# Performance work log

Measured on AMD Instinct MI355X. Metric: run time of the kernel, lower is better.

## Reference

```python
import jax, jax.numpy as jnp
import numpy as np


def setup_inputs() -> dict:
    key = jax.random.key(0)
    k1, k2, k3 = jax.random.split(key, 3)
    x = jax.random.normal(k1, (32, 256, 32, 32), dtype=jnp.float32)
    weight = jax.random.normal(k2, (256, 256, 3, 3), dtype=jnp.float32) * 0.05
    bias = jax.random.normal(k3, (256,), dtype=jnp.float32) * 0.01
    return {"x": x, "weight": weight, "bias": bias}


def _forward(x, weight, bias):
    B, cin, n, _ = x.shape
    cout, _, k, _ = weight.shape
    s = (k - 1) // 2
    nf = n // 2 + 1
    bins = n * nf

    # fft shift matrix: exp(-1j*2*pi*s*(i+j)/n), kept rfft columns
    idx = jnp.arange(n)
    shift = idx[None, :] + idx[:, None]                     # (n, n)
    shift_m = jnp.exp(-1j * 2 * jnp.pi * s * shift / n)[:, :nf]
    shift_m = shift_m.reshape(bins, 1, 1).astype(jnp.complex64)

    # xfft: (B, cin, n, nf) -> (bins, cin, B)
    xfft = jnp.fft.rfft2(x)
    xfft = jnp.transpose(xfft, (2, 3, 1, 0)).reshape(bins, cin, B)

    # Hfft: (cout, cin, n, nf) -> (bins, cout, cin), shifted + conj
    Hfft = jnp.fft.rfft2(weight, s=(n, n)).reshape(cout, cin, bins)
    Hfft = shift_m * jnp.conj(jnp.transpose(Hfft, (2, 0, 1)))

    def sq_abs(z):
        return jnp.real(z) ** 2 + jnp.imag(z) ** 2

    RowNorm = jnp.sqrt(jnp.sum(sq_abs(Hfft), axis=2))       # (bins, cout)
    ColNorm = jnp.sqrt(jnp.sum(sq_abs(Hfft), axis=1))       # (bins, cin)

    if cout >= cin:
        RowLoss = jnp.mean((RowNorm - jnp.sqrt(cin / cout)) ** 2)
        ColLoss = jnp.mean((ColNorm - 1.0) ** 2)
        HHT = jnp.einsum('npc,nqc->npq', jnp.conj(Hfft), Hfft)  # (bins, cout, cout)
        mask = jnp.triu(jnp.ones((cout, cout), bool), k=1)
        count = bins * (cout * (cout - 1) // 2)
        AngLoss = jnp.sum(sq_abs(HHT) * mask[None]) / count   # MSE(|HHT[triu]|, 0)
        L = cout * ColLoss + cin * RowLoss + AngLoss
    else:
        RowLoss = jnp.mean((RowNorm - 1.0) ** 2)
        ColLoss = jnp.mean((ColNorm - jnp.sqrt(cout / cin)) ** 2)
        HTH = jnp.einsum('ndp,ndq->npq', jnp.conj(Hfft), Hfft)  # (bins, cin, cin)
        mask = jnp.triu(jnp.ones((cin, cin), bool), k=1)
        count = bins * (cin * (cin - 1) // 2)
        AngLoss = jnp.sum(sq_abs(HTH) * mask[None]) / count
        L = cout * ColLoss + cin * RowLoss + AngLoss

    # per-bin complex matmul: (bins, cout, cin) @ (bins, cin, B) -> (bins, cout, B)
    yfft = Hfft @ xfft
    yfft = jnp.transpose(yfft.reshape(n, nf, cout, B), (3, 2, 0, 1))  # (B, cout, n, nf)
    y = jnp.fft.irfft2(yfft, s=(n, n))
    y = y + bias[None, :, None, None]
    return y, L


def reference(x, weight, bias):
    return _forward(x, weight, bias)
```

## Files before the change

kernel.cpp:

```cpp
#include <hip/hip_runtime.h>
#include <math.h>

typedef __attribute__((ext_vector_type(8)))  short  short8;
typedef __attribute__((ext_vector_type(16))) float  float16;

#define TWO_PI_OVER_32 0.19634954084936207f

static __device__ __forceinline__ unsigned short f2bf(float f) {
    unsigned int u = __float_as_uint(f);
    u = (u + 0x7FFFu + ((u >> 16) & 1u)) >> 16;
    return (unsigned short)u;
}
static __device__ __forceinline__ float bf2f(unsigned short s) {
    return __uint_as_float(((unsigned int)s) << 16);
}

static __device__ __forceinline__ void g2l16(const void* g, void* l) {
    __builtin_amdgcn_global_load_lds(
        (const __attribute__((address_space(1))) unsigned int*)g,
        (__attribute__((address_space(3))) unsigned int*)l, 16, 0, 0);
}

#define SBAR() do { __builtin_amdgcn_s_barrier(); \
                    __builtin_amdgcn_sched_barrier(0); } while (0)
#define WAITV(n) do { asm volatile("s_waitcnt vmcnt(" #n ")" ::: "memory"); \
                      __builtin_amdgcn_sched_barrier(0); } while (0)

__global__ __launch_bounds__(256) void k_prepx(const float* __restrict__ x,
                                               unsigned short* __restrict__ xb,
                                               const float* __restrict__ w,
                                               unsigned short* __restrict__ wt,
                                               unsigned short* __restrict__ Vb,
                                               float* __restrict__ Drow,
                                               float* __restrict__ Dcol) {
    int tid = threadIdx.x;
    if (blockIdx.x < 4096) {
        int g = blockIdx.x * 256 + tid;
        int c = g & 31, r = (g >> 5) & 31, cig = (g >> 10) & 31, b = g >> 15;
        const float* xp = x + ((b * 256 + cig * 8) * 32 + r) * 32 + c;
        union { unsigned short u[8]; uint4 v; } pk;
        #pragma unroll
        for (int u = 0; u < 8; ++u) pk.u[u] = f2bf(xp[u * 1024]);
        ((uint4*)xb)[g] = pk.v;
        return;
    }
    __shared__ float sdata[45];
    __shared__ float ws2[256 * 9];
    int blk = blockIdx.x - 4096, lane = tid & 63;
    bool colmode = blk >= 256;
    int pc = blk & 255;
    if (tid < 45) sdata[tid] = 0.f;

    int p = colmode ? tid : pc;
    int c = colmode ? pc : tid;
    float w9[9];
    #pragma unroll
    for (int t = 0; t < 9; ++t) w9[t] = w[(p * 256 + c) * 9 + t];
    if (!colmode) {
        #pragma unroll
        for (int t = 0; t < 9; ++t) ws2[tid * 9 + t] = w9[t];
    }
    __syncthreads();

    int idx = 0;
    for (int ta = 0; ta < 9; ++ta)
        for (int tb = ta; tb < 9; ++tb) {
            float v = w9[ta] * w9[tb];
            #pragma unroll
            for (int off = 32; off > 0; off >>= 1) v += __shfl_down(v, off);
            if (lane == 0) atomicAdd(&sdata[idx], v);
            ++idx;
        }
    __syncthreads();
    if (tid < 45) (colmode ? Dcol : Drow)[tid * 256 + pc] = sdata[tid];

    if (!colmode) {
        #pragma unroll
        for (int t = 0; t < 9; ++t)
            wt[t * 65536 + (c >> 3) * 2048 + p * 8 + (c & 7)] = f2bf(w9[t]);
        if (tid < 320) {
            int ta = tid >> 5, cig = tid & 31;
            union { unsigned short u[8]; uint4 v; } pk;
            #pragma unroll
            for (int u = 0; u < 8; ++u)
                pk.u[u] = (ta < 9) ? f2bf(ws2[(cig * 8 + u) * 9 + ta]) : (unsigned short)0;
            ((uint4*)Vb)[(p * 10 + ta) * 32 + cig] = pk.v;
        }
    }
}

__global__ __launch_bounds__(256, 3) void k_conv(const unsigned short* __restrict__ xb,
                                                 const unsigned short* __restrict__ wt,
                                                 const float* __restrict__ bias,
                                                 const unsigned short* __restrict__ Vb,
                                                 unsigned short* __restrict__ Gb,
                                                 float* __restrict__ y) {
    __shared__ unsigned short xs[640 * 8];
    __shared__ unsigned short wsm[2][1152 * 8];

    const int tid  = threadIdx.x;
    const int lane = tid & 63;
    const int half = lane >> 5;
    const int m    = lane & 31;

    if (blockIdx.x < 210) {
        int blk = blockIdx.x, I = 0;
        while (blk >= 20 - I) { blk -= 20 - I; ++I; }
        int J = I + blk;
        const int wave = tid >> 6;
        const int wm = wave >> 1, wn = wave & 1;
        const int row0 = I * 128 + wm * 64;
        const int col0 = J * 128 + wn * 64;

        float16 acc[2][2];
        #pragma unroll
        for (int i = 0; i < 2; ++i)
            #pragma unroll
            for (int j = 0; j < 2; ++j)
                #pragma unroll
                for (int r = 0; r < 16; ++r) acc[i][j][r] = 0.f;

        const short8* vb = (const short8*)Vb;
        for (int kc = 0; kc < 16; ++kc) {
            int cig = kc * 2 + half;
            short8 a0 = vb[(row0 + m) * 32 + cig];
            short8 a1 = vb[(row0 + 32 + m) * 32 + cig];
            short8 b0 = vb[(col0 + m) * 32 + cig];
            short8 b1 = vb[(col0 + 32 + m) * 32 + cig];
            acc[0][0] = __builtin_amdgcn_mfma_f32_32x32x16_bf16(a0, b0, acc[0][0], 0, 0, 0);
            acc[0][1] = __builtin_amdgcn_mfma_f32_32x32x16_bf16(a0, b1, acc[0][1], 0, 0, 0);
            acc[1][0] = __builtin_amdgcn_mfma_f32_32x32x16_bf16(a1, b0, acc[1][0], 0, 0, 0);
            acc[1][1] = __builtin_amdgcn_mfma_f32_32x32x16_bf16(a1, b1, acc[1][1], 0, 0, 0);
        }
        #pragma unroll
        for (int i = 0; i < 2; ++i)
            #pragma unroll
            for (int j = 0; j < 2; ++j)
                #pragma unroll
                for (int reg = 0; reg < 16; ++reg) {
                    int crow = (reg & 3) + 8 * (reg >> 2) + 4 * half;
                    Gb[(row0 + i * 32 + crow) * 2560 + col0 + j * 32 + m] =
                        f2bf(acc[i][j][reg]);
                }
        return;
    }

    const int wv    = tid >> 6;
    const int id    = blockIdx.x - 210;
    const int xcd   = id & 7;
    const int local = id >> 3;
    const int b     = xcd * 4 + (local >> 4);
    const int rem   = local & 15;
    const int co0   = (rem & 3) * 64;
    const int r0    = (rem >> 2) * 8;

    float16 acc[2][2];
    #pragma unroll
    for (int i = 0; i < 2; ++i)
        #pragma unroll
        for (int ns = 0; ns < 2; ++ns)
            #pragma unroll
            for (int r = 0; r < 16; ++r) acc[i][ns][r] = 0.f;

    const uint4* xbv = (const uint4*)xb;
    const uint4* wtv = (const uint4*)wt;

    const int cigl = lane >> 5;
    const int coll = lane & 31;

    auto stage_x = [&](int kc) {
        uint4* xd = (uint4*)xs;
        #pragma unroll
        for (int ch = wv; ch < 10; ch += 4) {
            int gr = (r0 + ch + 31) & 31;
            g2l16(&xbv[((b * 32 + kc * 2 + cigl) * 32 + gr) * 32 + coll],
                  &xd[ch * 64]);
        }
    };
    auto stage_w = [&](int buf, int kc) {
        uint4* wd = (uint4*)wsm[buf];
        #pragma unroll
        for (int wc = wv; wc < 18; wc += 4) {
            int t = wc >> 1, cig = wc & 1;
            g2l16(&wtv[t * 8192 + (kc * 2 + cig) * 256 + co0 + lane],
                  &wd[wc * 64]);
        }
    };

    auto compute = [&](int buf) {
        const short8* xsl = (const short8*)xs;
        const short8* wsl = (const short8*)wsm[buf];
        #pragma unroll
        for (int btv = 0; btv < 3; ++btv) {
            short8 a0[3], a1[3];
            #pragma unroll
            for (int atv = 0; atv < 3; ++atv) {
                int t = atv * 3 + btv;
                a0[atv] = wsl[(t * 2 + half) * 64 + m];
                a1[atv] = wsl[(t * 2 + half) * 64 + 32 + m];
            }
            #pragma unroll
            for (int s = 0; s < 4; ++s) {
                short8 bf = xsl[((wv * 2 + s) * 2 + half) * 32 + ((m + btv + 31) & 31)];
                #pragma unroll
                for (int atv = 0; atv < 3; ++atv) {
                    int ns = s - atv;
                    if (ns >= 0 && ns < 2) {
                        acc[0][ns] = __builtin_amdgcn_mfma_f32_32x32x16_bf16(a0[atv], bf, acc[0][ns], 0, 0, 0);
                        acc[1][ns] = __builtin_amdgcn_mfma_f32_32x32x16_bf16(a1[atv], bf, acc[1][ns], 0, 0, 0);
                    }
                }
            }
        }
    };

    stage_w(0, 0);
    stage_x(0);
    #pragma unroll 1
    for (int kc = 0; kc < 16; ++kc) {
        int buf = kc & 1;
        if (kc < 15) {
            stage_w(buf ^ 1, kc + 1);
            if (wv < 2) { WAITV(5); } else { WAITV(4); }
        } else {
            WAITV(0);
        }
        SBAR();
        __builtin_amdgcn_s_setprio(1);
        compute(buf);
        __builtin_amdgcn_s_setprio(0);
        SBAR();
        if (kc < 15) stage_x(kc + 1);
    }

    #pragma unroll
    for (int i = 0; i < 2; ++i) {
        #pragma unroll
        for (int ns = 0; ns < 2; ++ns) {
            int r = r0 + wv * 2 + ns;
            #pragma unroll
            for (int reg = 0; reg < 16; ++reg) {
                int crow = (reg & 3) + 8 * (reg >> 2) + 4 * half;
                int co = co0 + i * 32 + crow;
                y[(b * 256 + co) * 1024 + r * 32 + m] = acc[i][ns][reg] + bias[co];
            }
        }
    }
}

__global__ __launch_bounds__(256) void k_loss(const float* __restrict__ Drow,
                                              const float* __restrict__ Dcol,
                                              const unsigned short* __restrict__ Gb,
                                              float* __restrict__ rowp,
                                              float* __restrict__ colp,
                                              float* __restrict__ angp) {
    __shared__ union {
        struct { float coef[45]; float red[2]; } rc;
        struct { unsigned short gs[9 * 2560]; float red; } ang;
    } sh;
    int tid = threadIdx.x;

    if (blockIdx.x < 544) {
        int bin = blockIdx.x;
        int u = bin / 17, v = bin % 17;
        if (tid < 2) sh.rc.red[tid] = 0.f;
        if (tid < 45) {
            int idx = 0, TA = 0, TB = 0;
            for (int ta = 0; ta < 9; ++ta)
                for (int tb = ta; tb < 9; ++tb) {
                    if (idx == tid) { TA = ta; TB = tb; }
                    ++idx;
                }
            int da = TA / 3 - TB / 3;
            int db = TA % 3 - TB % 3;
            float cth = cosf(TWO_PI_OVER_32 * (float)(u * da + v * db));
            sh.rc.coef[tid] = (TA == TB) ? 1.f : 2.f * cth;
        }
        __syncthreads();

        float s1 = 0.f, s2 = 0.f;
        const float* dr = Drow + tid;
        const float* dc = Dcol + tid;
        #pragma unroll
        for (int i = 0; i < 45; ++i) {
            s1 += sh.rc.coef[i] * dr[i * 256];
            s2 += sh.rc.coef[i] * dc[i * 256];
        }
        float e1 = sqrtf(fmaxf(s1, 0.f)) - 1.f; e1 *= e1;
        float e2 = sqrtf(fmaxf(s2, 0.f)) - 1.f; e2 *= e2;
        #pragma unroll
        for (int off = 32; off > 0; off >>= 1) {
            e1 += __shfl_down(e1, off);
            e2 += __shfl_down(e2, off);
        }
        if ((tid & 63) == 0) { atomicAdd(&sh.rc.red[0], e1); atomicAdd(&sh.rc.red[1], e2); }
        __syncthreads();
        if (tid == 0) { rowp[bin] = sh.rc.red[0]; colp[bin] = sh.rc.red[1]; }
    } else {
        int p = blockIdx.x - 544;
        if (tid == 0) sh.ang.red = 0.f;
        uint4* gsv = (uint4*)sh.ang.gs;
        const uint4* gbv = (const uint4*)Gb;
        for (int i = tid; i < 2880; i += 256) {
            int rr = i / 320, cc = i - rr * 320;
            gsv[i] = gbv[(p * 10 + rr) * 320 + cc];
        }
        __syncthreads();

        int q = tid;
        float S = 0.f;
        if (q > p) {
            float g5[5][5];
            #pragma unroll
            for (int i = 0; i < 5; ++i)
                #pragma unroll
                for (int j = 0; j < 5; ++j) g5[i][j] = 0.f;
            #pragma unroll
            for (int ta = 0; ta < 9; ++ta)
                #pragma unroll
                for (int tb = 0; tb < 9; ++tb) {
                    float c = bf2f(sh.ang.gs[ta * 2560 + q * 10 + tb]);
                    g5[ta / 3 - tb / 3 + 2][ta % 3 - tb % 3 + 2] += c;
                }
            #pragma unroll
            for (int da = 0; da < 5; ++da) {
                const float* g = g5[da];
                float sq = g[0]*g[0] + g[1]*g[1] + g[2]*g[2] + g[3]*g[3] + g[4]*g[4];
                float cr = g[0]*g[2] + g[1]*g[3] + g[2]*g[4] + g[0]*g[4];
                S += 17.f * sq + 2.f * cr;
            }
            S *= 32.f;
        }
        #pragma unroll
        for (int off = 32; off > 0; off >>= 1) S += __shfl_down(S, off);
        if ((tid & 63) == 0) atomicAdd(&sh.ang.red, S);
        __syncthreads();
        if (tid == 0) angp[p] = sh.ang.red;
    }
}

__global__ __launch_bounds__(256) void k_fin(const float* __restrict__ rowp,
                                             const float* __restrict__ colp,
                                             const float* __restrict__ angp,
                                             float* __restrict__ out) {
    __shared__ float sred[3][4];
    int tid = threadIdx.x;
    float r = 0.f, c = 0.f, a = 0.f;
    for (int i = tid; i < 544; i += 256) { r += rowp[i]; c += colp[i]; }
    a = angp[tid];
    #pragma unroll
    for (int off = 32; off > 0; off >>= 1) {
        r += __shfl_down(r, off);
        c += __shfl_down(c, off);
        a += __shfl_down(a, off);
    }
    if ((tid & 63) == 0) {
        int wv = tid >> 6;
        sred[0][wv] = r; sred[1][wv] = c; sred[2][wv] = a;
    }
    __syncthreads();
    if (tid == 0) {
        float R = sred[0][0] + sred[0][1] + sred[0][2] + sred[0][3];
        float C = sred[1][0] + sred[1][1] + sred[1][2] + sred[1][3];
        float A = sred[2][0] + sred[2][1] + sred[2][2] + sred[2][3];
        out[8388608] = R / 544.f + C / 544.f + A / (544.f * 32640.f);
    }
}

extern "C" void kernel_launch(void* const* d_in, const int* in_sizes, int n_in,
                              void* d_out, int out_size, void* d_ws, size_t ws_size,
                              hipStream_t stream) {
    const float* x    = (const float*)d_in[0];
    const float* w    = (const float*)d_in[1];
    const float* bias = (const float*)d_in[2];
    float* out = (float*)d_out;

    char* ws = (char*)d_ws;
    unsigned short* wt = (unsigned short*)ws;
    unsigned short* xb = (unsigned short*)(ws + 1179648);
    unsigned short* Vb = (unsigned short*)(ws + 17956864);
    float* Drow  = (float*)(ws + 19267584);
    float* Dcol  = (float*)(ws + 19313664);
    float* rowp  = (float*)(ws + 19359744);
    float* colp  = (float*)(ws + 19361920);
    float* angp  = (float*)(ws + 19364096);
    unsigned short* Gb = (unsigned short*)(ws + 19392512);

    k_prepx <<<4608, 256, 0, stream>>>(x, xb, w, wt, Vb, Drow, Dcol);
    k_conv  <<<722, 256, 0, stream>>>(xb, wt, bias, Vb, Gb, out);
    k_loss  <<<800, 256, 0, stream>>>(Drow, Dcol, Gb, rowp, colp, angp);
    k_fin   <<<1, 256, 0, stream>>>(rowp, colp, angp, out);
}
```

Measured before the change: 154.6 us.

## Load conv input tiles directly into registers instead of staging through LDS

The direct-conv path no longer stages the input row tile in shared memory. Each wave now loads its 12 shifted bf16 input fragments straight from global memory into registers and prefetches the next K-chunk right after compute. The goal is to remove the LDS write/read traffic for x and free LDS for occupancy. The cost is 12 extra short8 registers per thread and redundant, possibly less coalesced global loads, since neighbouring waves fetch overlapping rows. The WAITV counts were tuned for the old x staging and were not updated.

```diff
diff --git a/kernel.cpp b/kernel.cpp
--- a/kernel.cpp
+++ b/kernel.cpp
@@ -95,7 +95,6 @@
                                                  const unsigned short* __restrict__ Vb,
                                                  unsigned short* __restrict__ Gb,
                                                  float* __restrict__ y) {
-    __shared__ unsigned short xs[640 * 8];
     __shared__ unsigned short wsm[2][1152 * 8];
 
     const int tid  = threadIdx.x;
@@ -162,21 +161,9 @@
             #pragma unroll
             for (int r = 0; r < 16; ++r) acc[i][ns][r] = 0.f;
 
-    const uint4* xbv = (const uint4*)xb;
-    const uint4* wtv = (const uint4*)wt;
-
-    const int cigl = lane >> 5;
-    const int coll = lane & 31;
-
-    auto stage_x = [&](int kc) {
-        uint4* xd = (uint4*)xs;
-        #pragma unroll
-        for (int ch = wv; ch < 10; ch += 4) {
-            int gr = (r0 + ch + 31) & 31;
-            g2l16(&xbv[((b * 32 + kc * 2 + cigl) * 32 + gr) * 32 + coll],
-                  &xd[ch * 64]);
-        }
-    };
+    const uint4*  wtv = (const uint4*)wt;
+    const short8* xg  = (const short8*)xb;
+
     auto stage_w = [&](int buf, int kc) {
         uint4* wd = (uint4*)wsm[buf];
         #pragma unroll
@@ -187,35 +174,41 @@
         }
     };
 
+    short8 xr[12];
+    auto loadx = [&](int kc) {
+        #pragma unroll
+        for (int btv = 0; btv < 3; ++btv) {
+            int gc = (m + btv + 31) & 31;
+            #pragma unroll
+            for (int s = 0; s < 4; ++s) {
+                int gr = (r0 + wv * 2 + s + 31) & 31;
+                xr[btv * 4 + s] =
+                    xg[((b * 32 + kc * 2 + half) * 32 + gr) * 32 + gc];
+            }
+        }
+    };
+
     auto compute = [&](int buf) {
-        const short8* xsl = (const short8*)xs;
         const short8* wsl = (const short8*)wsm[buf];
         #pragma unroll
-        for (int btv = 0; btv < 3; ++btv) {
-            short8 a0[3], a1[3];
+        for (int btv = 0; btv < 3; ++btv)
             #pragma unroll
             for (int atv = 0; atv < 3; ++atv) {
                 int t = atv * 3 + btv;
-                a0[atv] = wsl[(t * 2 + half) * 64 + m];
-                a1[atv] = wsl[(t * 2 + half) * 64 + 32 + m];
-            }
-            #pragma unroll
-            for (int s = 0; s < 4; ++s) {
-                short8 bf = xsl[((wv * 2 + s) * 2 + half) * 32 + ((m + btv + 31) & 31)];
-                #pragma unroll
-                for (int atv = 0; atv < 3; ++atv) {
-                    int ns = s - atv;
-                    if (ns >= 0 && ns < 2) {
-                        acc[0][ns] = __builtin_amdgcn_mfma_f32_32x32x16_bf16(a0[atv], bf, acc[0][ns], 0, 0, 0);
-                        acc[1][ns] = __builtin_amdgcn_mfma_f32_32x32x16_bf16(a1[atv], bf, acc[1][ns], 0, 0, 0);
+                #pragma unroll
+                for (int i = 0; i < 2; ++i) {
+                    short8 a = wsl[(t * 2 + half) * 64 + i * 32 + m];
+                    #pragma unroll
+                    for (int ns = 0; ns < 2; ++ns) {
+                        acc[i][ns] = __builtin_amdgcn_mfma_f32_32x32x16_bf16(
+                            a, xr[btv * 4 + atv + ns], acc[i][ns], 0, 0, 0);
                     }
                 }
             }
-        }
     };
 
     stage_w(0, 0);
-    stage_x(0);
+    loadx(0);
     #pragma unroll 1
     for (int kc = 0; kc < 16; ++kc) {
         int buf = kc & 1;
@@ -229,8 +222,8 @@
         __builtin_amdgcn_s_setprio(1);
         compute(buf);
         __builtin_amdgcn_s_setprio(0);
+        if (kc < 15) loadx(kc + 1);
         SBAR();
-        if (kc < 15) stage_x(kc + 1);
     }
 
     #pragma unroll
```

Result: slower. 158.7 us (+2.7%).

## Fuse fp32-to-bf16 input conversion into conv kernel's register-staged x loads

Applied to the files above, without the earlier changes.

Drops the separate pass in k_prepx that converted x to a bf16 workspace copy. k_conv now loads fp32 x tiles into registers one step ahead, converts and packs them to bf16, and writes them into shared memory after compute. This removes a full write and re-read of the converted activation tensor, but each conv block now reads twice as many bytes of x, puts more pressure on registers, and adds an LDS-write wait before each barrier.

```diff
diff --git a/kernel.cpp b/kernel.cpp
--- a/kernel.cpp
+++ b/kernel.cpp
@@ -25,28 +25,19 @@
                     __builtin_amdgcn_sched_barrier(0); } while (0)
 #define WAITV(n) do { asm volatile("s_waitcnt vmcnt(" #n ")" ::: "memory"); \
                       __builtin_amdgcn_sched_barrier(0); } while (0)
-
-__global__ __launch_bounds__(256) void k_prepx(const float* __restrict__ x,
-                                               unsigned short* __restrict__ xb,
-                                               const float* __restrict__ w,
+#define WAITLGKM0() do { asm volatile("s_waitcnt lgkmcnt(0)" ::: "memory"); \
+                         __builtin_amdgcn_sched_barrier(0); } while (0)
+#define SCHED_FENCE() __builtin_amdgcn_sched_barrier(0)
+
+__global__ __launch_bounds__(256) void k_prepx(const float* __restrict__ w,
                                                unsigned short* __restrict__ wt,
                                                unsigned short* __restrict__ Vb,
                                                float* __restrict__ Drow,
                                                float* __restrict__ Dcol) {
-    int tid = threadIdx.x;
-    if (blockIdx.x < 4096) {
-        int g = blockIdx.x * 256 + tid;
-        int c = g & 31, r = (g >> 5) & 31, cig = (g >> 10) & 31, b = g >> 15;
-        const float* xp = x + ((b * 256 + cig * 8) * 32 + r) * 32 + c;
-        union { unsigned short u[8]; uint4 v; } pk;
-        #pragma unroll
-        for (int u = 0; u < 8; ++u) pk.u[u] = f2bf(xp[u * 1024]);
-        ((uint4*)xb)[g] = pk.v;
-        return;
-    }
     __shared__ float sdata[45];
     __shared__ float ws2[256 * 9];
-    int blk = blockIdx.x - 4096, lane = tid & 63;
+    int tid = threadIdx.x;
+    int blk = blockIdx.x, lane = tid & 63;
     bool colmode = blk >= 256;
     int pc = blk & 255;
     if (tid < 45) sdata[tid] = 0.f;
@@ -89,7 +80,7 @@
     }
 }
 
-__global__ __launch_bounds__(256, 3) void k_conv(const unsigned short* __restrict__ xb,
+__global__ __launch_bounds__(256, 3) void k_conv(const float* __restrict__ xf,
                                                  const unsigned short* __restrict__ wt,
                                                  const float* __restrict__ bias,
                                                  const unsigned short* __restrict__ Vb,
@@ -162,21 +153,11 @@
             #pragma unroll
             for (int r = 0; r < 16; ++r) acc[i][ns][r] = 0.f;
 
-    const uint4* xbv = (const uint4*)xb;
     const uint4* wtv = (const uint4*)wt;
 
     const int cigl = lane >> 5;
-    const int coll = lane & 31;
-
-    auto stage_x = [&](int kc) {
-        uint4* xd = (uint4*)xs;
-        #pragma unroll
-        for (int ch = wv; ch < 10; ch += 4) {
-            int gr = (r0 + ch + 31) & 31;
-            g2l16(&xbv[((b * 32 + kc * 2 + cigl) * 32 + gr) * 32 + coll],
-                  &xd[ch * 64]);
-        }
-    };
+    const int cnt  = (tid < 128) ? 3 : 2;
+
     auto stage_w = [&](int buf, int kc) {
         uint4* wd = (uint4*)wsm[buf];
         #pragma unroll
@@ -184,6 +165,44 @@
             int t = wc >> 1, cig = wc & 1;
             g2l16(&wtv[t * 8192 + (kc * 2 + cig) * 256 + co0 + lane],
                   &wd[wc * 64]);
+        }
+    };
+
+    float4 xlo[3], xhi[3];
+    auto load_x = [&](int kc) {
+        #pragma unroll
+        for (int j = 0; j < 3; ++j) {
+            if (j < cnt) {
+                int idg  = (j < 2) ? (tid + 256 * j) : (512 + tid);
+                int slot = idg >> 6, sub = idg & 63;
+                int cig  = sub >> 5, s32 = sub & 31;
+                int u2   = s32 >> 3, cq = s32 & 7;
+                int gr   = (r0 + slot + 31) & 31;
+                const float* p = xf + ((size_t)(b * 256 + kc * 16 + cig * 8 + 2 * u2)) * 1024
+                               + gr * 32 + cq * 4;
+                xlo[j] = *(const float4*)p;
+                xhi[j] = *(const float4*)(p + 1024);
+            }
+        }
+    };
+    auto cvt_x = [&]() {
+        unsigned int* xw = (unsigned int*)xs;
+        #pragma unroll
+        for (int j = 0; j < 3; ++j) {
+            if (j < cnt) {
+                int idg  = (j < 2) ? (tid + 256 * j) : (512 + tid);
+                int slot = idg >> 6, sub = idg & 63;
+                int cig  = sub >> 5, s32 = sub & 31;
+                int u2   = s32 >> 3, cq = s32 & 7;
+                const float* lp = (const float*)&xlo[j];
+                const float* hp = (const float*)&xhi[j];
+                #pragma unroll
+                for (int e = 0; e < 4; ++e) {
+                    unsigned int pk = (unsigned int)f2bf(lp[e]) |
+                                      ((unsigned int)f2bf(hp[e]) << 16);
+                    xw[((slot * 2 + cig) * 32 + cq * 4 + e) * 4 + u2] = pk;
+                }
+            }
         }
     };
 
@@ -215,22 +234,28 @@
     };
 
     stage_w(0, 0);
-    stage_x(0);
+    SCHED_FENCE();
+    load_x(0);
+    SCHED_FENCE();
+    cvt_x();
     #pragma unroll 1
     for (int kc = 0; kc < 16; ++kc) {
         int buf = kc & 1;
         if (kc < 15) {
+            load_x(kc + 1);
+            SCHED_FENCE();
             stage_w(buf ^ 1, kc + 1);
-            if (wv < 2) { WAITV(5); } else { WAITV(4); }
+            if (wv < 2) { WAITV(11); } else { WAITV(8); }
         } else {
             WAITV(0);
         }
+        WAITLGKM0();
         SBAR();
         __builtin_amdgcn_s_setprio(1);
         compute(buf);
         __builtin_amdgcn_s_setprio(0);
         SBAR();
-        if (kc < 15) stage_x(kc + 1);
+        if (kc < 15) cvt_x();
     }
 
     #pragma unroll
@@ -377,17 +402,16 @@
 
     char* ws = (char*)d_ws;
     unsigned short* wt = (unsigned short*)ws;
-    unsigned short* xb = (unsigned short*)(ws + 1179648);
-    unsigned short* Vb = (unsigned short*)(ws + 17956864);
-    float* Drow  = (float*)(ws + 19267584);
-    float* Dcol  = (float*)(ws + 19313664);
-    float* rowp  = (float*)(ws + 19359744);
-    float* colp  = (float*)(ws + 19361920);
-    float* angp  = (float*)(ws + 19364096);
-    unsigned short* Gb = (unsigned short*)(ws + 19392512);
-
-    k_prepx <<<4608, 256, 0, stream>>>(x, xb, w, wt, Vb, Drow, Dcol);
-    k_conv  <<<722, 256, 0, stream>>>(xb, wt, bias, Vb, Gb, out);
+    unsigned short* Vb = (unsigned short*)(ws + 1179648);
+    float* Drow  = (float*)(ws + 2490368);
+    float* Dcol  = (float*)(ws + 2536448);
+    float* rowp  = (float*)(ws + 2582528);
+    float* colp  = (float*)(ws + 2584704);
+    float* angp  = (float*)(ws + 2586880);
+    unsigned short* Gb = (unsigned short*)(ws + 2588672);
+
+    k_prepx <<<512, 256, 0, stream>>>(w, wt, Vb, Drow, Dcol);
+    k_conv  <<<722, 256, 0, stream>>>(x, wt, bias, Vb, Gb, out);
     k_loss  <<<800, 256, 0, stream>>>(Drow, Dcol, Gb, rowp, colp, angp);
     k_fin   <<<1, 256, 0, stream>>>(rowp, colp, angp, out);
 }
```

Result: no change. 154.6 us (-0.1%).
